# Optimization experiments

Measured on AMD Instinct MI355X. Metric: run time of the kernel, lower is better.

## Reference

```python
import jax, jax.numpy as jnp
import numpy as np

BS, C, C2, H, W = 8, 256, 128, 64, 64

def setup_inputs() -> dict:
    key = jax.random.key(0)
    ks = jax.random.split(key, 9)
    s = 0.05
    return {
        "appearance_1": jax.random.normal(ks[0], (BS, C2, H, W), jnp.float32),
        "appearance_2": jax.random.normal(ks[1], (BS, C2, H, W), jnp.float32),
        "motion": jax.random.normal(ks[2], (BS, C, H, W), jnp.float32),
        "Wq": jax.random.normal(ks[3], (C2, C2), jnp.float32) * s,
        "bq": jax.random.normal(ks[4], (C2,), jnp.float32) * s,
        "Wk": jax.random.normal(ks[5], (C2, C2), jnp.float32) * s,
        "bk": jax.random.normal(ks[6], (C2,), jnp.float32) * s,
        "Wv": jax.random.normal(ks[7], (C, C), jnp.float32) * s,
        "bv": jax.random.normal(ks[8], (C,), jnp.float32) * s,
    }

def reference(appearance_1, appearance_2, motion, Wq, bq, Wk, bk, Wv, bv):
    bs, c, h, w = motion.shape
    n = h * w
    a1 = appearance_1.reshape(bs, -1, n)   # [b, C2, N]
    a2 = appearance_2.reshape(bs, -1, n)   # [b, C2, N]
    m = motion.reshape(bs, c, n)           # [b, C,  N]
    # 1x1 convs == per-pixel linear projections
    q = jnp.einsum('oc,bcn->bon', Wq, a2) + bq[None, :, None]  # [b, C2, N]
    k = jnp.einsum('oc,bcn->bon', Wk, a1) + bk[None, :, None]  # [b, C2, N]
    v = jnp.einsum('oc,bcn->bon', Wv, m) + bv[None, :, None]   # [b, C,  N]
    # energy[b, i, j] = <q[:, i], k[:, j]> ; softmax over j
    energy = jnp.einsum('bci,bcj->bij', q, k)                  # [b, N, N]
    attention = jax.nn.softmax(energy, axis=-1)
    # out = V @ attention^T
    out = jnp.einsum('bcj,bij->bci', v, attention)             # [b, C, N]
    out = out.reshape(bs, c, h, w)
    fuse_out = out * motion
    return (fuse_out, out)
```

## Files before the change

kernel.cpp:

```cpp
#include <hip/hip_runtime.h>
#include <cstdint>
#include <cstddef>

#define BS   8
#define C    256
#define C2   128
#define NPIX 4096

typedef unsigned short u16;
typedef unsigned int   u32;
typedef __bf16 bf16_t;
typedef bf16_t bf16x8 __attribute__((ext_vector_type(8)));
typedef float  f32x16 __attribute__((ext_vector_type(16)));

__device__ __forceinline__ u16 f2bf(float f) {
    union { float ff; u32 i; } x; x.ff = f;
    u32 r = x.i + 0x7fffu + ((x.i >> 16) & 1u);
    return (u16)(r >> 16);
}

__device__ __forceinline__ void split2(float f, u16& hi, u16& lo) {
    union { float ff; u32 i; } x; x.ff = f;
    hi = (u16)(x.i >> 16);
    union { u32 i; float ff; } h; h.i = x.i & 0xffff0000u;
    union { float ff; u32 i; } r; r.ff = f - h.ff;
    lo = (u16)(r.i >> 16);
}

__device__ __forceinline__ u32 pk2(u16 a, u16 b) { return (u32)a | ((u32)b << 16); }

__global__ __launch_bounds__(256)
void prep_w(const float* __restrict__ Wq, const float* __restrict__ Wk,
            const float* __restrict__ Wv,
            u16* __restrict__ qh, u16* __restrict__ ql,
            u16* __restrict__ kh, u16* __restrict__ kl,
            u16* __restrict__ vh, u16* __restrict__ vl) {
    const int z = blockIdx.y;
    const int O = (z == 2) ? C : C2;
    const int npair = O * O / 8;
    const int idx = blockIdx.x * 256 + threadIdx.x;
    if (idx >= npair) return;
    const int o  = idx & (O - 1);
    const int c8 = idx >> ((z == 2) ? 8 : 7);
    const float* src = (z == 0) ? Wq : (z == 1) ? Wk : Wv;
    u16* oh = (z == 0) ? qh : (z == 1) ? kh : vh;
    u16* ol = (z == 0) ? ql : (z == 1) ? kl : vl;
    const float4 f0 = *(const float4*)(src + (size_t)o * O + c8 * 8);
    const float4 f1 = *(const float4*)(src + (size_t)o * O + c8 * 8 + 4);
    u16 h[8], l[8];
    split2(f0.x, h[0], l[0]); split2(f0.y, h[1], l[1]);
    split2(f0.z, h[2], l[2]); split2(f0.w, h[3], l[3]);
    split2(f1.x, h[4], l[4]); split2(f1.y, h[5], l[5]);
    split2(f1.z, h[6], l[6]); split2(f1.w, h[7], l[7]);
    *(uint4*)(oh + (size_t)idx * 8) =
        make_uint4(pk2(h[0], h[1]), pk2(h[2], h[3]), pk2(h[4], h[5]), pk2(h[6], h[7]));
    *(uint4*)(ol + (size_t)idx * 8) =
        make_uint4(pk2(l[0], l[1]), pk2(l[2], l[3]), pk2(l[4], l[5]), pk2(l[6], l[7]));
}

__global__ __launch_bounds__(256, 2)
void proj_qk2(const u16* __restrict__ qh2, const u16* __restrict__ ql2,
              const float* __restrict__ bq,
              const u16* __restrict__ kh2, const u16* __restrict__ kl2,
              const float* __restrict__ bk,
              const float* __restrict__ a2, const float* __restrict__ a1,
              u16* __restrict__ qout, u16* __restrict__ kout) {
    __shared__ __align__(16) u16 Xb[2][16][64][8];
    const int t  = threadIdx.x;
    const int w  = t >> 6;
    const int li = t & 31;
    const int hs = (t >> 5) & 1;
    const int n0 = blockIdx.x * 64;
    const int b  = blockIdx.y;
    const int z  = blockIdx.z;

    const u16* wh  = z ? kh2 : qh2;
    const u16* wl  = z ? kl2 : ql2;
    const float* bias = z ? bk : bq;
    const float* x = z ? a1 : a2;
    u16* out = z ? kout : qout;

    {
        const int sn = t & 63;
        const float* xb = x + (size_t)b * C2 * NPIX + n0 + sn;
        float xv[4][8];
        #pragma unroll
        for (int q = 0; q < 4; ++q) {
            const int c0 = (q * 4 + w) * 8;
            #pragma unroll
            for (int j = 0; j < 8; ++j) xv[q][j] = xb[(size_t)(c0 + j) * NPIX];
        }
        #pragma unroll
        for (int q = 0; q < 4; ++q) {
            u16 h[8], l[8];
            #pragma unroll
            for (int j = 0; j < 8; ++j) split2(xv[q][j], h[j], l[j]);
            *(uint4*)&Xb[0][q * 4 + w][sn][0] =
                make_uint4(pk2(h[0], h[1]), pk2(h[2], h[3]), pk2(h[4], h[5]), pk2(h[6], h[7]));
            *(uint4*)&Xb[1][q * 4 + w][sn][0] =
                make_uint4(pk2(l[0], l[1]), pk2(l[2], l[3]), pk2(l[4], l[5]), pk2(l[6], l[7]));
        }
    }
    __syncthreads();

    f32x16 acc[2];
    #pragma unroll
    for (int nt = 0; nt < 2; ++nt)
        #pragma unroll
        for (int e = 0; e < 16; ++e) acc[nt][e] = 0.f;

    const int ob = w * 32 + li;
    #pragma unroll
    for (int ks = 0; ks < 8; ++ks) {
        const int c8 = ks * 2 + hs;
        const bf16x8 bh = *(const bf16x8*)(wh + ((size_t)c8 * C2 + ob) * 8);
        const bf16x8 bl = *(const bf16x8*)(wl + ((size_t)c8 * C2 + ob) * 8);
        #pragma unroll
        for (int nt = 0; nt < 2; ++nt) {
            const bf16x8 ah = *(const bf16x8*)&Xb[0][c8][nt * 32 + li][0];
            const bf16x8 al = *(const bf16x8*)&Xb[1][c8][nt * 32 + li][0];
            acc[nt] = __builtin_amdgcn_mfma_f32_32x32x16_bf16(ah, bh, acc[nt], 0, 0, 0);
            acc[nt] = __builtin_amdgcn_mfma_f32_32x32x16_bf16(ah, bl, acc[nt], 0, 0, 0);
            acc[nt] = __builtin_amdgcn_mfma_f32_32x32x16_bf16(al, bh, acc[nt], 0, 0, 0);
        }
    }

    const float bb = bias[ob];
    #pragma unroll
    for (int nt = 0; nt < 2; ++nt)
        #pragma unroll
        for (int r = 0; r < 16; ++r) {
            const int n = n0 + nt * 32 + (r & 3) + 8 * (r >> 2) + 4 * hs;
            out[((size_t)b * NPIX + n) * C2 + ob] = f2bf(acc[nt][r] + bb);
        }
}

__global__ __launch_bounds__(256, 2)
void proj_v2(const u16* __restrict__ wh, const u16* __restrict__ wl,
             const float* __restrict__ bias,
             const float* __restrict__ x,
             u16* __restrict__ out) {
    __shared__ __align__(16) u16 Xb[2][32][64][8];
    const int t  = threadIdx.x;
    const int w  = t >> 6;
    const int li = t & 31;
    const int hs = (t >> 5) & 1;
    const int n0 = blockIdx.x * 64;
    const int b  = blockIdx.y;

    {
        const int sn = t & 63;
        const float* xb = x + (size_t)b * C * NPIX + n0 + sn;
        #pragma unroll
        for (int rr = 0; rr < 2; ++rr) {
            float xv[4][8];
            #pragma unroll
            for (int q = 0; q < 4; ++q) {
                const int c0 = ((rr * 4 + q) * 4 + w) * 8;
                #pragma unroll
                for (int j = 0; j < 8; ++j) xv[q][j] = xb[(size_t)(c0 + j) * NPIX];
            }
            #pragma unroll
            for (int q = 0; q < 4; ++q) {
                u16 h[8], l[8];
                #pragma unroll
                for (int j = 0; j < 8; ++j) split2(xv[q][j], h[j], l[j]);
                const int c8 = (rr * 4 + q) * 4 + w;
                *(uint4*)&Xb[0][c8][sn][0] =
                    make_uint4(pk2(h[0], h[1]), pk2(h[2], h[3]), pk2(h[4], h[5]), pk2(h[6], h[7]));
                *(uint4*)&Xb[1][c8][sn][0] =
                    make_uint4(pk2(l[0], l[1]), pk2(l[2], l[3]), pk2(l[4], l[5]), pk2(l[6], l[7]));
            }
        }
    }
    __syncthreads();

    f32x16 acc[2][2];
    #pragma unroll
    for (int ot = 0; ot < 2; ++ot)
        #pragma unroll
        for (int nt = 0; nt < 2; ++nt)
            #pragma unroll
            for (int e = 0; e < 16; ++e) acc[ot][nt][e] = 0.f;

    #pragma unroll
    for (int ks = 0; ks < 16; ++ks) {
        const int c8 = ks * 2 + hs;
        bf16x8 ah[2], al[2], xh[2], xl[2];
        #pragma unroll
        for (int ot = 0; ot < 2; ++ot) {
            const int o = w * 64 + ot * 32 + li;
            ah[ot] = *(const bf16x8*)(wh + ((size_t)c8 * C + o) * 8);
            al[ot] = *(const bf16x8*)(wl + ((size_t)c8 * C + o) * 8);
        }
        #pragma unroll
        for (int nt = 0; nt < 2; ++nt) {
            xh[nt] = *(const bf16x8*)&Xb[0][c8][nt * 32 + li][0];
            xl[nt] = *(const bf16x8*)&Xb[1][c8][nt * 32 + li][0];
        }
        #pragma unroll
        for (int ot = 0; ot < 2; ++ot)
            #pragma unroll
            for (int nt = 0; nt < 2; ++nt) {
                acc[ot][nt] = __builtin_amdgcn_mfma_f32_32x32x16_bf16(ah[ot], xh[nt], acc[ot][nt], 0, 0, 0);
                acc[ot][nt] = __builtin_amdgcn_mfma_f32_32x32x16_bf16(ah[ot], xl[nt], acc[ot][nt], 0, 0, 0);
                acc[ot][nt] = __builtin_amdgcn_mfma_f32_32x32x16_bf16(al[ot], xh[nt], acc[ot][nt], 0, 0, 0);
            }
    }

    #pragma unroll
    for (int ot = 0; ot < 2; ++ot)
        #pragma unroll
        for (int nt = 0; nt < 2; ++nt)
            #pragma unroll
            for (int g = 0; g < 4; ++g) {
                const int orow = w * 64 + ot * 32 + 8 * g + 4 * hs;
                const float4 b4 = *(const float4*)&bias[orow];
                const size_t base = ((size_t)b * C + orow) * NPIX + n0 + nt * 32 + li;
                out[base]            = f2bf(acc[ot][nt][g * 4 + 0] + b4.x);
                out[base + NPIX]     = f2bf(acc[ot][nt][g * 4 + 1] + b4.y);
                out[base + 2 * NPIX] = f2bf(acc[ot][nt][g * 4 + 2] + b4.z);
                out[base + 3 * NPIX] = f2bf(acc[ot][nt][g * 4 + 3] + b4.w);
            }
}

struct SR { uint4 k[2]; uint4 v[4]; };

__device__ __forceinline__ void stg_load(const u16* __restrict__ kg,
                                         const u16* __restrict__ vg,
                                         int jt, int t, SR& R) {
    const u16* kp = kg + (size_t)jt * 32 * 128;
    #pragma unroll
    for (int q = 0; q < 2; ++q)
        R.k[q] = *(const uint4*)(kp + (size_t)(t + 256 * q) * 8);
    const u16* vp = vg + jt * 32 + (t & 3) * 8;
    #pragma unroll
    for (int q = 0; q < 4; ++q)
        R.v[q] = *(const uint4*)(vp + (size_t)((t >> 2) + 64 * q) * NPIX);
}

__device__ __forceinline__ void stg_write(u16* __restrict__ kb, u16* __restrict__ vb,
                                          int t, const SR& R) {
    #pragma unroll
    for (int q = 0; q < 2; ++q) {
        const int idx = t + 256 * q;
        const int row = idx >> 4;
        const int ch  = (idx & 15) ^ (row & 15);
        *(uint4*)(kb + row * 128 + ch * 8) = R.k[q];
    }
    #pragma unroll
    for (int q = 0; q < 4; ++q) {
        const int c   = (t >> 2) + 64 * q;
        const int rc  = c >> 1;
        const int q8  = (c & 1) * 8 + (t & 3) * 2;
        const int x   = rc & 15;
        const int ch0 = q8 ^ x;
        const int ch1 = (q8 + 1) ^ x;
        *(uint2*)(vb + rc * 64 + ch0 * 4) = make_uint2(R.v[q].x, R.v[q].y);
        *(uint2*)(vb + rc * 64 + ch1 * 4) = make_uint2(R.v[q].z, R.v[q].w);
    }
}

__global__ __launch_bounds__(256, 2)
void attn_mfma3(const u16* __restrict__ qt,
                const u16* __restrict__ kt,
                const u16* __restrict__ vn,
                float* __restrict__ opart0,
                float* __restrict__ opart1,
                float* __restrict__ sbuf) {
    __shared__ u16 Kb[2][32 * 128];
    __shared__ u16 Vb[2][128 * 64];

    const int t  = threadIdx.x;
    const int w  = t >> 6;
    const int li = t & 31;
    const int hs = (t >> 5) & 1;

    const int b  = blockIdx.x & 7;
    const int it = (blockIdx.x >> 3) & 31;
    const int h  = blockIdx.x >> 8;
    const int i0 = it * 128;
    const int iw = i0 + w * 32 + li;
    const int j0 = h * 2048;

    bf16x8 qf[8];
    {
        const u16* qp = qt + ((size_t)b * NPIX + iw) * C2 + hs * 8;
        #pragma unroll
        for (int ct = 0; ct < 8; ++ct) qf[ct] = *(const bf16x8*)(qp + ct * 16);
    }

    f32x16 oacc[8];
    #pragma unroll
    for (int ct = 0; ct < 8; ++ct)
        #pragma unroll
        for (int e = 0; e < 16; ++e) oacc[ct][e] = 0.f;

    const u16* ktb = kt + ((size_t)b * NPIX + j0) * C2;
    const u16* vnb = vn + (size_t)b * C * NPIX + j0;

    SR R;
    stg_load(ktb, vnb, 0, t, R);
    stg_write(&Kb[0][0], &Vb[0][0], t, R);
    stg_load(ktb, vnb, 1, t, R);
    __syncthreads();

    float ssl = 0.f;
    for (int itr = 0; itr < 64; ++itr) {
        const int cur = itr & 1;
        if (itr < 63) {
            stg_write(&Kb[cur ^ 1][0], &Vb[cur ^ 1][0], t, R);
            if (itr < 62) stg_load(ktb, vnb, itr + 2, t, R);
        }
        const u16* kb = &Kb[cur][0];
        const u16* vb = &Vb[cur][0];

        f32x16 s;
        #pragma unroll
        for (int e = 0; e < 16; ++e) s[e] = 0.f;
        {
            const int xr = li & 15;
            #pragma unroll
            for (int ct = 0; ct < 8; ++ct) {
                const int ch = (ct * 2 + hs) ^ xr;
                const bf16x8 kf = *(const bf16x8*)(kb + li * 128 + ch * 8);
                s = __builtin_amdgcn_mfma_f32_32x32x16_bf16(kf, qf[ct], s, 0, 0, 0);
            }
        }

        u32 pk[8];
        #pragma unroll
        for (int n = 0; n < 8; ++n) {
            const float p0 = __expf(s[2 * n]);
            const float p1 = __expf(s[2 * n + 1]);
            ssl += p0 + p1;
            pk[n] = (u32)f2bf(p0) | ((u32)f2bf(p1) << 16);
        }

        bf16x8 pf[2];
        #pragma unroll
        for (int seg = 0; seg < 2; ++seg) {
            const u32 A0 = pk[4 * seg + 0], A1 = pk[4 * seg + 1];
            const u32 A2 = pk[4 * seg + 2], A3 = pk[4 * seg + 3];
            const u32 own0 = hs ? A2 : A0, own1 = hs ? A3 : A1;
            const u32 snd0 = hs ? A0 : A2, snd1 = hs ? A1 : A3;
            const u32 rcv0 = (u32)__shfl_xor((int)snd0, 32, 64);
            const u32 rcv1 = (u32)__shfl_xor((int)snd1, 32, 64);
            union { u32 u[4]; bf16x8 v; } bb;
            bb.u[0] = hs ? rcv0 : own0;
            bb.u[1] = hs ? rcv1 : own1;
            bb.u[2] = hs ? own0 : rcv0;
            bb.u[3] = hs ? own1 : rcv1;
            pf[seg] = bb.v;
        }

        #pragma unroll
        for (int ct = 0; ct < 8; ++ct) {
            const int c  = ct * 32 + li;
            const int rc = c >> 1;
            const int x  = rc & 15;
            const u16* vr = vb + rc * 64;
            const int cb = (c & 1) * 8 + hs * 2;
            #pragma unroll
            for (int seg = 0; seg < 2; ++seg) {
                const int q8  = cb + seg * 4;
                const int ch0 = q8 ^ x;
                const int ch1 = (q8 + 1) ^ x;
                union { uint2 g[2]; bf16x8 v8; } u;
                u.g[0] = *(const uint2*)(vr + ch0 * 4);
                u.g[1] = *(const uint2*)(vr + ch1 * 4);
                oacc[ct] = __builtin_amdgcn_mfma_f32_32x32x16_bf16(u.v8, pf[seg], oacc[ct], 0, 0, 0);
            }
        }
        __syncthreads();
    }

    ssl += __shfl_xor(ssl, 32, 64);
    if (hs == 0) sbuf[((size_t)h * BS + b) * NPIX + iw] = ssl;

    float* op = h ? opart1 : opart0;
    #pragma unroll
    for (int ct = 0; ct < 8; ++ct) {
        #pragma unroll
        for (int r = 0; r < 16; ++r) {
            const int c = ct * 32 + (r & 3) + 8 * (r >> 2) + 4 * hs;
            op[((size_t)b * C + c) * NPIX + iw] = oacc[ct][r];
        }
    }
}

__global__ __launch_bounds__(256)
void attn_merge(float* __restrict__ fuse,
                float* __restrict__ outp,
                const float* __restrict__ motion,
                const float* __restrict__ sbuf) {
    const size_t idx = ((size_t)blockIdx.x * 256 + threadIdx.x) * 4;
    const int n = (int)(idx & (NPIX - 1));
    const int b = (int)(idx >> 20);
    const float4 o1 = *(const float4*)(fuse + idx);
    const float4 o2 = *(const float4*)(outp + idx);
    const float4 sa = *(const float4*)(sbuf + (size_t)b * NPIX + n);
    const float4 sb = *(const float4*)(sbuf + (size_t)(BS + b) * NPIX + n);
    float4 o;
    o.x = (o1.x + o2.x) / (sa.x + sb.x);
    o.y = (o1.y + o2.y) / (sa.y + sb.y);
    o.z = (o1.z + o2.z) / (sa.z + sb.z);
    o.w = (o1.w + o2.w) / (sa.w + sb.w);
    const float4 mv = *(const float4*)(motion + idx);
    *(float4*)(outp + idx) = o;
    *(float4*)(fuse + idx) = make_float4(o.x * mv.x, o.y * mv.y, o.z * mv.z, o.w * mv.w);
}

extern "C" void kernel_launch(void* const* d_in, const int* in_sizes, int n_in,
                              void* d_out, int out_size, void* d_ws, size_t ws_size,
                              hipStream_t stream) {
    const float* a1     = (const float*)d_in[0];
    const float* a2     = (const float*)d_in[1];
    const float* motion = (const float*)d_in[2];
    const float* Wq = (const float*)d_in[3];
    const float* bq = (const float*)d_in[4];
    const float* Wk = (const float*)d_in[5];
    const float* bk = (const float*)d_in[6];
    const float* Wv = (const float*)d_in[7];
    const float* bv = (const float*)d_in[8];

    float* outp = (float*)d_out;
    float* slot0 = outp;
    float* slot1 = outp + (size_t)BS * C * NPIX;

    u16* qws = (u16*)d_ws;
    u16* kws = qws + (size_t)BS * C2 * NPIX;
    u16* vws = kws + (size_t)BS * C2 * NPIX;
    float* sbuf = (float*)(vws + (size_t)BS * C * NPIX);
    u16* wqh = (u16*)(sbuf + (size_t)2 * BS * NPIX);
    u16* wql = wqh + C2 * C2;
    u16* wkh = wql + C2 * C2;
    u16* wkl = wkh + C2 * C2;
    u16* wvh = wkl + C2 * C2;
    u16* wvl = wvh + C * C;

    const dim3 blk(256);
    prep_w<<<dim3(32, 3), blk, 0, stream>>>(Wq, Wk, Wv, wqh, wql, wkh, wkl, wvh, wvl);
    proj_qk2<<<dim3(NPIX / 64, BS, 2), blk, 0, stream>>>(
        wqh, wql, bq, wkh, wkl, bk, a2, a1, qws, kws);
    proj_v2<<<dim3(NPIX / 64, BS), blk, 0, stream>>>(wvh, wvl, bv, motion, vws);

    attn_mfma3<<<dim3(512), blk, 0, stream>>>(qws, kws, vws, slot0, slot1, sbuf);

    attn_merge<<<dim3((BS * C * NPIX) / 1024), blk, 0, stream>>>(
        slot0, slot1, motion, sbuf);
}
```

Before: 329.7 us.

## Merge Q/K/V projections into one kernel with two-term bf16 split and MFMA priority hints

The separate Q/K and V projection kernels become a single launch with four z-slices. The V path now uses 32-pixel tiles and a smaller LDS footprint, which allows more blocks per CU. Activations are converted to a single bf16 instead of a hi/lo pair, which drops one of the three MFMAs per step, and weights now split with round-to-nearest hi plus residual. The attention kernel wraps its MFMA loops in s_setprio hints and packs probabilities with native bf16 casts. Cost: lower precision in the projections, since activation rounding error is no longer compensated.

```diff
diff --git a/kernel.cpp b/kernel.cpp
--- a/kernel.cpp
+++ b/kernel.cpp
@@ -18,15 +18,9 @@
     u32 r = x.i + 0x7fffu + ((x.i >> 16) & 1u);
     return (u16)(r >> 16);
 }
-
-__device__ __forceinline__ void split2(float f, u16& hi, u16& lo) {
-    union { float ff; u32 i; } x; x.ff = f;
-    hi = (u16)(x.i >> 16);
-    union { u32 i; float ff; } h; h.i = x.i & 0xffff0000u;
-    union { float ff; u32 i; } r; r.ff = f - h.ff;
-    lo = (u16)(r.i >> 16);
-}
-
+__device__ __forceinline__ float bf2f(u16 h) {
+    union { u32 i; float f; } x; x.i = (u32)h << 16; return x.f;
+}
 __device__ __forceinline__ u32 pk2(u16 a, u16 b) { return (u32)a | ((u32)b << 16); }
 
 __global__ __launch_bounds__(256)
@@ -45,183 +39,139 @@
     const float* src = (z == 0) ? Wq : (z == 1) ? Wk : Wv;
     u16* oh = (z == 0) ? qh : (z == 1) ? kh : vh;
     u16* ol = (z == 0) ? ql : (z == 1) ? kl : vl;
-    const float4 f0 = *(const float4*)(src + (size_t)o * O + c8 * 8);
-    const float4 f1 = *(const float4*)(src + (size_t)o * O + c8 * 8 + 4);
     u16 h[8], l[8];
-    split2(f0.x, h[0], l[0]); split2(f0.y, h[1], l[1]);
-    split2(f0.z, h[2], l[2]); split2(f0.w, h[3], l[3]);
-    split2(f1.x, h[4], l[4]); split2(f1.y, h[5], l[5]);
-    split2(f1.z, h[6], l[6]); split2(f1.w, h[7], l[7]);
+    #pragma unroll
+    for (int j = 0; j < 8; ++j) {
+        const float f = src[(size_t)o * O + c8 * 8 + j];
+        h[j] = f2bf(f);
+        l[j] = f2bf(f - bf2f(h[j]));
+    }
     *(uint4*)(oh + (size_t)idx * 8) =
         make_uint4(pk2(h[0], h[1]), pk2(h[2], h[3]), pk2(h[4], h[5]), pk2(h[6], h[7]));
     *(uint4*)(ol + (size_t)idx * 8) =
         make_uint4(pk2(l[0], l[1]), pk2(l[2], l[3]), pk2(l[4], l[5]), pk2(l[6], l[7]));
 }
 
-__global__ __launch_bounds__(256, 2)
-void proj_qk2(const u16* __restrict__ qh2, const u16* __restrict__ ql2,
-              const float* __restrict__ bq,
-              const u16* __restrict__ kh2, const u16* __restrict__ kl2,
-              const float* __restrict__ bk,
+__global__ __launch_bounds__(256, 4)
+void proj_all(const u16* __restrict__ wqh, const u16* __restrict__ wql,
+              const u16* __restrict__ wkh, const u16* __restrict__ wkl,
+              const u16* __restrict__ wvh, const u16* __restrict__ wvl,
+              const float* __restrict__ bq, const float* __restrict__ bk,
+              const float* __restrict__ bv,
               const float* __restrict__ a2, const float* __restrict__ a1,
-              u16* __restrict__ qout, u16* __restrict__ kout) {
-    __shared__ __align__(16) u16 Xb[2][16][64][8];
+              const float* __restrict__ motion,
+              u16* __restrict__ qout, u16* __restrict__ kout,
+              u16* __restrict__ vout) {
+    __shared__ __align__(16) u16 Xb[16][64][8];
     const int t  = threadIdx.x;
     const int w  = t >> 6;
     const int li = t & 31;
     const int hs = (t >> 5) & 1;
-    const int n0 = blockIdx.x * 64;
+    const int z  = blockIdx.z;
     const int b  = blockIdx.y;
-    const int z  = blockIdx.z;
-
-    const u16* wh  = z ? kh2 : qh2;
-    const u16* wl  = z ? kl2 : ql2;
-    const float* bias = z ? bk : bq;
-    const float* x = z ? a1 : a2;
-    u16* out = z ? kout : qout;
-
-    {
-        const int sn = t & 63;
-        const float* xb = x + (size_t)b * C2 * NPIX + n0 + sn;
-        float xv[4][8];
-        #pragma unroll
-        for (int q = 0; q < 4; ++q) {
-            const int c0 = (q * 4 + w) * 8;
-            #pragma unroll
-            for (int j = 0; j < 8; ++j) xv[q][j] = xb[(size_t)(c0 + j) * NPIX];
-        }
-        #pragma unroll
-        for (int q = 0; q < 4; ++q) {
-            u16 h[8], l[8];
-            #pragma unroll
-            for (int j = 0; j < 8; ++j) split2(xv[q][j], h[j], l[j]);
-            *(uint4*)&Xb[0][q * 4 + w][sn][0] =
-                make_uint4(pk2(h[0], h[1]), pk2(h[2], h[3]), pk2(h[4], h[5]), pk2(h[6], h[7]));
-            *(uint4*)&Xb[1][q * 4 + w][sn][0] =
-                make_uint4(pk2(l[0], l[1]), pk2(l[2], l[3]), pk2(l[4], l[5]), pk2(l[6], l[7]));
-        }
-    }
-    __syncthreads();
-
-    f32x16 acc[2];
-    #pragma unroll
-    for (int nt = 0; nt < 2; ++nt)
-        #pragma unroll
-        for (int e = 0; e < 16; ++e) acc[nt][e] = 0.f;
-
-    const int ob = w * 32 + li;
-    #pragma unroll
-    for (int ks = 0; ks < 8; ++ks) {
-        const int c8 = ks * 2 + hs;
-        const bf16x8 bh = *(const bf16x8*)(wh + ((size_t)c8 * C2 + ob) * 8);
-        const bf16x8 bl = *(const bf16x8*)(wl + ((size_t)c8 * C2 + ob) * 8);
-        #pragma unroll
-        for (int nt = 0; nt < 2; ++nt) {
-            const bf16x8 ah = *(const bf16x8*)&Xb[0][c8][nt * 32 + li][0];
-            const bf16x8 al = *(const bf16x8*)&Xb[1][c8][nt * 32 + li][0];
-            acc[nt] = __builtin_amdgcn_mfma_f32_32x32x16_bf16(ah, bh, acc[nt], 0, 0, 0);
-            acc[nt] = __builtin_amdgcn_mfma_f32_32x32x16_bf16(ah, bl, acc[nt], 0, 0, 0);
-            acc[nt] = __builtin_amdgcn_mfma_f32_32x32x16_bf16(al, bh, acc[nt], 0, 0, 0);
-        }
-    }
-
-    const float bb = bias[ob];
-    #pragma unroll
-    for (int nt = 0; nt < 2; ++nt)
-        #pragma unroll
-        for (int r = 0; r < 16; ++r) {
-            const int n = n0 + nt * 32 + (r & 3) + 8 * (r >> 2) + 4 * hs;
-            out[((size_t)b * NPIX + n) * C2 + ob] = f2bf(acc[nt][r] + bb);
-        }
-}
-
-__global__ __launch_bounds__(256, 2)
-void proj_v2(const u16* __restrict__ wh, const u16* __restrict__ wl,
-             const float* __restrict__ bias,
-             const float* __restrict__ x,
-             u16* __restrict__ out) {
-    __shared__ __align__(16) u16 Xb[2][32][64][8];
-    const int t  = threadIdx.x;
-    const int w  = t >> 6;
-    const int li = t & 31;
-    const int hs = (t >> 5) & 1;
-    const int n0 = blockIdx.x * 64;
-    const int b  = blockIdx.y;
-
-    {
-        const int sn = t & 63;
-        const float* xb = x + (size_t)b * C * NPIX + n0 + sn;
-        #pragma unroll
-        for (int rr = 0; rr < 2; ++rr) {
-            float xv[4][8];
+
+    if (z < 2) {
+        const u16* wh = z ? wkh : wqh;
+        const u16* wl = z ? wkl : wql;
+        const float* bias = z ? bk : bq;
+        const float* x    = z ? a1 : a2;
+        u16* out          = z ? kout : qout;
+        const int n0 = blockIdx.x * 64;
+        {
+            const int sn = t & 63;
+            const float* xb = x + (size_t)b * C2 * NPIX + n0 + sn;
             #pragma unroll
             for (int q = 0; q < 4; ++q) {
-                const int c0 = ((rr * 4 + q) * 4 + w) * 8;
+                const int c8 = q * 4 + w;
+                union { bf16_t e[8]; uint4 u4; } cv;
                 #pragma unroll
-                for (int j = 0; j < 8; ++j) xv[q][j] = xb[(size_t)(c0 + j) * NPIX];
-            }
-            #pragma unroll
-            for (int q = 0; q < 4; ++q) {
-                u16 h[8], l[8];
+                for (int j = 0; j < 8; ++j)
+                    cv.e[j] = (bf16_t)xb[(size_t)(c8 * 8 + j) * NPIX];
+                *(uint4*)&Xb[c8][sn][0] = cv.u4;
+            }
+        }
+        __syncthreads();
+
+        f32x16 acc[2];
+        #pragma unroll
+        for (int nt = 0; nt < 2; ++nt)
+            #pragma unroll
+            for (int e = 0; e < 16; ++e) acc[nt][e] = 0.f;
+
+        const int ob = w * 32 + li;
+        #pragma unroll
+        for (int ks = 0; ks < 8; ++ks) {
+            const int c8 = ks * 2 + hs;
+            const bf16x8 bh = *(const bf16x8*)(wh + ((size_t)c8 * C2 + ob) * 8);
+            const bf16x8 bl = *(const bf16x8*)(wl + ((size_t)c8 * C2 + ob) * 8);
+            #pragma unroll
+            for (int nt = 0; nt < 2; ++nt) {
+                const bf16x8 a = *(const bf16x8*)&Xb[c8][nt * 32 + li][0];
+                acc[nt] = __builtin_amdgcn_mfma_f32_32x32x16_bf16(a, bh, acc[nt], 0, 0, 0);
+                acc[nt] = __builtin_amdgcn_mfma_f32_32x32x16_bf16(a, bl, acc[nt], 0, 0, 0);
+            }
+        }
+
+        const float bb = bias[ob];
+        #pragma unroll
+        for (int nt = 0; nt < 2; ++nt)
+            #pragma unroll
+            for (int r = 0; r < 16; ++r) {
+                const int n = n0 + nt * 32 + (r & 3) + 8 * (r >> 2) + 4 * hs;
+                out[((size_t)b * NPIX + n) * C2 + ob] = f2bf(acc[nt][r] + bb);
+            }
+    } else {
+        u16 (*Xv)[32][8] = (u16 (*)[32][8])(&Xb[0][0][0]);
+        const int n0 = blockIdx.x * 64 + (z - 2) * 32;
+        {
+            const int sn = t & 31;
+            const int cg = t >> 5;
+            const float* xb = motion + (size_t)b * C * NPIX + n0 + sn;
+            #pragma unroll
+            for (int r = 0; r < 4; ++r) {
+                const int c8 = r * 8 + cg;
+                union { bf16_t e[8]; uint4 u4; } cv;
                 #pragma unroll
-                for (int j = 0; j < 8; ++j) split2(xv[q][j], h[j], l[j]);
-                const int c8 = (rr * 4 + q) * 4 + w;
-                *(uint4*)&Xb[0][c8][sn][0] =
-                    make_uint4(pk2(h[0], h[1]), pk2(h[2], h[3]), pk2(h[4], h[5]), pk2(h[6], h[7]));
-                *(uint4*)&Xb[1][c8][sn][0] =
-                    make_uint4(pk2(l[0], l[1]), pk2(l[2], l[3]), pk2(l[4], l[5]), pk2(l[6], l[7]));
-            }
-        }
-    }
-    __syncthreads();
-
-    f32x16 acc[2][2];
-    #pragma unroll
-    for (int ot = 0; ot < 2; ++ot)
-        #pragma unroll
-        for (int nt = 0; nt < 2; ++nt)
-            #pragma unroll
-            for (int e = 0; e < 16; ++e) acc[ot][nt][e] = 0.f;
-
-    #pragma unroll
-    for (int ks = 0; ks < 16; ++ks) {
-        const int c8 = ks * 2 + hs;
-        bf16x8 ah[2], al[2], xh[2], xl[2];
-        #pragma unroll
-        for (int ot = 0; ot < 2; ++ot) {
-            const int o = w * 64 + ot * 32 + li;
-            ah[ot] = *(const bf16x8*)(wh + ((size_t)c8 * C + o) * 8);
-            al[ot] = *(const bf16x8*)(wl + ((size_t)c8 * C + o) * 8);
-        }
-        #pragma unroll
-        for (int nt = 0; nt < 2; ++nt) {
-            xh[nt] = *(const bf16x8*)&Xb[0][c8][nt * 32 + li][0];
-            xl[nt] = *(const bf16x8*)&Xb[1][c8][nt * 32 + li][0];
-        }
+                for (int j = 0; j < 8; ++j)
+                    cv.e[j] = (bf16_t)xb[(size_t)(c8 * 8 + j) * NPIX];
+                *(uint4*)&Xv[c8][sn][0] = cv.u4;
+            }
+        }
+        __syncthreads();
+
+        f32x16 acc[2];
         #pragma unroll
         for (int ot = 0; ot < 2; ++ot)
             #pragma unroll
-            for (int nt = 0; nt < 2; ++nt) {
-                acc[ot][nt] = __builtin_amdgcn_mfma_f32_32x32x16_bf16(ah[ot], xh[nt], acc[ot][nt], 0, 0, 0);
-                acc[ot][nt] = __builtin_amdgcn_mfma_f32_32x32x16_bf16(ah[ot], xl[nt], acc[ot][nt], 0, 0, 0);
-                acc[ot][nt] = __builtin_amdgcn_mfma_f32_32x32x16_bf16(al[ot], xh[nt], acc[ot][nt], 0, 0, 0);
-            }
-    }
-
-    #pragma unroll
-    for (int ot = 0; ot < 2; ++ot)
-        #pragma unroll
-        for (int nt = 0; nt < 2; ++nt)
+            for (int e = 0; e < 16; ++e) acc[ot][e] = 0.f;
+
+        #pragma unroll
+        for (int ks = 0; ks < 16; ++ks) {
+            const int c8 = ks * 2 + hs;
+            const bf16x8 xf = *(const bf16x8*)&Xv[c8][li][0];
+            #pragma unroll
+            for (int ot = 0; ot < 2; ++ot) {
+                const int o = w * 64 + ot * 32 + li;
+                const bf16x8 ah = *(const bf16x8*)(wvh + ((size_t)c8 * C + o) * 8);
+                const bf16x8 al = *(const bf16x8*)(wvl + ((size_t)c8 * C + o) * 8);
+                acc[ot] = __builtin_amdgcn_mfma_f32_32x32x16_bf16(ah, xf, acc[ot], 0, 0, 0);
+                acc[ot] = __builtin_amdgcn_mfma_f32_32x32x16_bf16(al, xf, acc[ot], 0, 0, 0);
+            }
+        }
+
+        #pragma unroll
+        for (int ot = 0; ot < 2; ++ot)
             #pragma unroll
             for (int g = 0; g < 4; ++g) {
                 const int orow = w * 64 + ot * 32 + 8 * g + 4 * hs;
-                const float4 b4 = *(const float4*)&bias[orow];
-                const size_t base = ((size_t)b * C + orow) * NPIX + n0 + nt * 32 + li;
-                out[base]            = f2bf(acc[ot][nt][g * 4 + 0] + b4.x);
-                out[base + NPIX]     = f2bf(acc[ot][nt][g * 4 + 1] + b4.y);
-                out[base + 2 * NPIX] = f2bf(acc[ot][nt][g * 4 + 2] + b4.z);
-                out[base + 3 * NPIX] = f2bf(acc[ot][nt][g * 4 + 3] + b4.w);
-            }
+                const float4 b4 = *(const float4*)&bv[orow];
+                const size_t base = ((size_t)b * C + orow) * NPIX + n0 + li;
+                vout[base]            = f2bf(acc[ot][g * 4 + 0] + b4.x);
+                vout[base + NPIX]     = f2bf(acc[ot][g * 4 + 1] + b4.y);
+                vout[base + 2 * NPIX] = f2bf(acc[ot][g * 4 + 2] + b4.z);
+                vout[base + 3 * NPIX] = f2bf(acc[ot][g * 4 + 3] + b4.w);
+            }
+    }
 }
 
 struct SR { uint4 k[2]; uint4 v[4]; };
@@ -320,12 +270,14 @@
         for (int e = 0; e < 16; ++e) s[e] = 0.f;
         {
             const int xr = li & 15;
+            __builtin_amdgcn_s_setprio(1);
             #pragma unroll
             for (int ct = 0; ct < 8; ++ct) {
                 const int ch = (ct * 2 + hs) ^ xr;
                 const bf16x8 kf = *(const bf16x8*)(kb + li * 128 + ch * 8);
                 s = __builtin_amdgcn_mfma_f32_32x32x16_bf16(kf, qf[ct], s, 0, 0, 0);
             }
+            __builtin_amdgcn_s_setprio(0);
         }
 
         u32 pk[8];
@@ -334,7 +286,10 @@
             const float p0 = __expf(s[2 * n]);
             const float p1 = __expf(s[2 * n + 1]);
             ssl += p0 + p1;
-            pk[n] = (u32)f2bf(p0) | ((u32)f2bf(p1) << 16);
+            union { bf16_t e[2]; u32 u; } cv;
+            cv.e[0] = (bf16_t)p0;
+            cv.e[1] = (bf16_t)p1;
+            pk[n] = cv.u;
         }
 
         bf16x8 pf[2];
@@ -354,6 +309,7 @@
             pf[seg] = bb.v;
         }
 
+        __builtin_amdgcn_s_setprio(1);
         #pragma unroll
         for (int ct = 0; ct < 8; ++ct) {
             const int c  = ct * 32 + li;
@@ -372,6 +328,7 @@
                 oacc[ct] = __builtin_amdgcn_mfma_f32_32x32x16_bf16(u.v8, pf[seg], oacc[ct], 0, 0, 0);
             }
         }
+        __builtin_amdgcn_s_setprio(0);
         __syncthreads();
     }
 
@@ -441,9 +398,8 @@
 
     const dim3 blk(256);
     prep_w<<<dim3(32, 3), blk, 0, stream>>>(Wq, Wk, Wv, wqh, wql, wkh, wkl, wvh, wvl);
-    proj_qk2<<<dim3(NPIX / 64, BS, 2), blk, 0, stream>>>(
-        wqh, wql, bq, wkh, wkl, bk, a2, a1, qws, kws);
-    proj_v2<<<dim3(NPIX / 64, BS), blk, 0, stream>>>(wvh, wvl, bv, motion, vws);
+    proj_all<<<dim3(NPIX / 64, BS, 4), blk, 0, stream>>>(
+        wqh, wql, wkh, wkl, wvh, wvl, bq, bk, bv, a2, a1, motion, qws, kws, vws);
 
     attn_mfma3<<<dim3(512), blk, 0, stream>>>(qws, kws, vws, slot0, slot1, sbuf);
 
```

Result: faster. 302.3 us (-8.3%).
